# Performance work log

Measured on AMD Instinct MI355X. Metric: run time of the kernel, lower is better.

## Reference

```python
import jax, jax.numpy as jnp
import numpy as np

B, S, D = 2, 1024, 4096          # batch, prefill seqlen, model dim
H, KVH, HD = 32, 8, 128          # q heads, kv heads, head dim
MAX = 2048                       # kv-cache capacity
THETA = 1000000.0
REP = H // KVH


def _rope_tables(pos):
    # pos: [S] int -> cos/sin [S, HD]
    inv_freq = 1.0 / (THETA ** (jnp.arange(0, HD, 2, dtype=jnp.float32) / HD))
    freqs = pos[:, None].astype(jnp.float32) * inv_freq[None, :]
    emb = jnp.concatenate([freqs, freqs], axis=-1)
    return jnp.cos(emb), jnp.sin(emb)


def _rotate_half(t):
    t1, t2 = jnp.split(t, 2, axis=-1)
    return jnp.concatenate([-t2, t1], axis=-1)


def setup_inputs() -> dict:
    key = jax.random.key(0)
    k = jax.random.split(key, 8)
    sc = 1.0 / np.sqrt(D)
    x = jax.random.normal(k[0], (B, S, D), jnp.float32)
    storage_idx = jnp.arange(S, dtype=jnp.int32)
    cache = jnp.zeros((2, 1, B, KVH, MAX, HD), jnp.float32)
    causal = jnp.tril(jnp.ones((MAX, MAX), bool))
    mask = jnp.where(causal, 0.0, -1e9).astype(jnp.float32)
    Wq = jax.random.normal(k[1], (D, H * HD), jnp.float32) * sc
    bq = jax.random.normal(k[2], (H * HD,), jnp.float32) * 0.01
    Wk = jax.random.normal(k[3], (D, KVH * HD), jnp.float32) * sc
    bk = jax.random.normal(k[4], (KVH * HD,), jnp.float32) * 0.01
    Wv = jax.random.normal(k[5], (D, KVH * HD), jnp.float32) * sc
    bv = jax.random.normal(k[6], (KVH * HD,), jnp.float32) * 0.01
    Wo = jax.random.normal(k[7], (H * HD, D), jnp.float32) * sc
    return {"x": x, "storage_idx": storage_idx, "cache": cache, "mask": mask,
            "Wq": Wq, "bq": bq, "Wk": Wk, "bk": bk, "Wv": Wv, "bv": bv, "Wo": Wo}


def reference(x, storage_idx, cache, mask, Wq, bq, Wk, bk, Wv, bv, Wo):
    bsz, seqlen, _ = x.shape
    # QKV projections -> [b, heads, s, hd]
    xq = (x @ Wq + bq).reshape(bsz, seqlen, H, HD).transpose(0, 2, 1, 3)
    xk = (x @ Wk + bk).reshape(bsz, seqlen, KVH, HD).transpose(0, 2, 1, 3)
    xv = (x @ Wv + bv).reshape(bsz, seqlen, KVH, HD).transpose(0, 2, 1, 3)
    # inline RoPE at positions storage_idx
    cos, sin = _rope_tables(storage_idx)       # [s, hd]
    cos = cos[None, None]                      # [1,1,s,hd]
    sin = sin[None, None]
    xq = xq * cos + _rotate_half(xq) * sin
    xk = xk * cos + _rotate_half(xk) * sin
    # KV-cache scatter (index_copy_ on dim -2 at storage_idx)
    keys = cache[0, 0].at[:, :, storage_idx, :].set(xk)    # [b, kvh, MAX, hd]
    values = cache[1, 0].at[:, :, storage_idx, :].set(xv)
    # GQA: repeat kv heads
    keys = jnp.repeat(keys, REP, axis=1)       # [b, H, MAX, hd]
    values = jnp.repeat(values, REP, axis=1)
    # attention with additive mask rows gathered at storage_idx
    scores = jnp.einsum('bhqd,bhkd->bhqk', xq, keys) / np.sqrt(HD)
    scores = scores + mask[storage_idx][None, None]        # [b, H, s, MAX]
    attn = jax.nn.softmax(scores, axis=-1)
    out = jnp.einsum('bhqk,bhkd->bhqd', attn, values)
    out = out.transpose(0, 2, 1, 3).reshape(bsz, seqlen, H * HD)
    return out @ Wo
```

## Files before the change

kernel.cpp:

```cpp
#include <hip/hip_runtime.h>
#include <hip/hip_bf16.h>

typedef unsigned short u16;
typedef unsigned int   u32;
using bf16x8 = __attribute__((ext_vector_type(8))) short;
using f32x4  = __attribute__((ext_vector_type(4))) float;

#define AS1 __attribute__((address_space(1)))
#define AS3 __attribute__((address_space(3)))

static constexpr int S_   = 1024;
static constexpr int D_   = 4096;
static constexpr int H_   = 32;
static constexpr int KVH_ = 8;
static constexpr int HD_  = 128;
static constexpr int NQKV = H_*HD_ + 2*KVH_*HD_;

__device__ __forceinline__ u16 f2bf(float f) {
  union { float f; u32 u; } v; v.f = f;
  u32 r = v.u + 0x7FFFu + ((v.u >> 16) & 1u);
  return (u16)(r >> 16);
}

__global__ void k_convert(const float* __restrict__ src, u16* __restrict__ dst, int n4) {
  int i = blockIdx.x * blockDim.x + threadIdx.x;
  if (i >= n4) return;
  float4 v = ((const float4*)src)[i];
  ushort4 o;
  o.x = f2bf(v.x); o.y = f2bf(v.y); o.z = f2bf(v.z); o.w = f2bf(v.w);
  ((ushort4*)dst)[i] = o;
}

__global__ void k_transpose_w(const float* __restrict__ src, u16* __restrict__ dst,
                              int K, int N) {
  __shared__ float t[32][33];
  int k0 = blockIdx.y * 32, n0 = blockIdx.x * 32;
  int tx = threadIdx.x, ty = threadIdx.y;
#pragma unroll
  for (int i = 0; i < 4; ++i)
    t[ty + i*8][tx] = src[(size_t)(k0 + ty + i*8) * N + n0 + tx];
  __syncthreads();
#pragma unroll
  for (int i = 0; i < 4; ++i)
    dst[(size_t)(n0 + ty + i*8) * K + k0 + tx] = f2bf(t[tx][ty + i*8]);
}

__global__ void k_transpose_v(const u16* __restrict__ src, u16* __restrict__ dst) {
  __shared__ u16 t[32][33];
  int bg = blockIdx.z;
  int s0 = blockIdx.x * 32, h0 = blockIdx.y * 32;
  src += (size_t)bg * S_ * HD_;
  dst += (size_t)bg * S_ * HD_;
  int tx = threadIdx.x, ty = threadIdx.y;
#pragma unroll
  for (int i = 0; i < 4; ++i)
    t[ty + i*8][tx] = src[(size_t)(s0 + ty + i*8) * HD_ + h0 + tx];
  __syncthreads();
#pragma unroll
  for (int i = 0; i < 4; ++i)
    dst[(size_t)(h0 + ty + i*8) * S_ + s0 + tx] = t[tx][ty + i*8];
}

__global__ void k_rope(const int* __restrict__ sidx, float* __restrict__ cosd,
                       float* __restrict__ sind) {
  int i = blockIdx.x * blockDim.x + threadIdx.x;
  int s = i >> 6, d = i & 63;
  float pos  = (float)sidx[s];
  float invf = expf(-0.21586735246819178f * (float)d);
  float ph   = pos * invf;
  cosd[i] = cosf(ph);
  sind[i] = sinf(ph);
}

#define BAR   __builtin_amdgcn_s_barrier()
#define SCHB  __builtin_amdgcn_sched_barrier(0)

__global__ __launch_bounds__(512, 2) void k_gemmq(
    const u16* __restrict__ A, const u16* __restrict__ Bt,
    const float* __restrict__ bq, const float* __restrict__ bk,
    const float* __restrict__ bv,
    const float* __restrict__ cosd, const float* __restrict__ sind,
    u16* __restrict__ qb, u16* __restrict__ kb, u16* __restrict__ vb)
{
  constexpr int K = 4096;
  constexpr int ABYT = 256*128, BBYT = 256*128, STEP = ABYT+BBYT;
  __shared__ __align__(16) char lds[2*STEP];

  const int cpx = (int)gridDim.x >> 3;
  const int wkid = ((int)blockIdx.x & 7)*cpx + ((int)blockIdx.x >> 3);
  const int NT = 24;
  const int m0 = (wkid / NT) * 256, n0 = (wkid % NT) * 256;
  const int tid = threadIdx.x, w = tid>>6, lane = tid&63;
  const int l15 = lane&15, l4 = lane>>4;
  const int wr = w>>1, wc = w&1;
  const int row0 = tid>>3;
  const int ss = (tid&7) ^ (row0&7);
  const int NK = K >> 6;

  f32x4 acc[4][8];
#pragma unroll
  for (int i = 0; i < 4; ++i)
#pragma unroll
    for (int j = 0; j < 8; ++j) acc[i][j] = (f32x4){0.f,0.f,0.f,0.f};

  bf16x8 af[2][2][2];
  bf16x8 bfr[2][4][2];

#define QCHUNK(kt_, part_, r0c_)                                              \
  __builtin_amdgcn_global_load_lds(                                           \
    (AS1 void*)(((part_) ? Bt + (size_t)(n0 + (r0c_) + row0)*K                \
                         : A  + (size_t)(m0 + (r0c_) + row0)*K)               \
                + (size_t)(kt_)*64 + ss*8),                                   \
    (AS3 void*)(lds + ((kt_)&1)*STEP + (part_)*ABYT + (r0c_)*128 + w*1024),   \
    16, 0, 0)

#define QR_A(mh_, lA_)                                                        \
  _Pragma("unroll") for (int i2 = 0; i2 < 2; ++i2)                            \
  _Pragma("unroll") for (int kk = 0; kk < 2; ++kk) {                          \
    int row = wr*64 + ((mh_)*2 + i2)*16 + l15;                                \
    af[mh_][i2][kk] = *(const bf16x8*)((lA_) + row*128 + (((kk*4+l4) ^ (row&7)) << 4)); }

#define QR_B(nh_, lB_)                                                        \
  _Pragma("unroll") for (int jj = 0; jj < 4; ++jj)                            \
  _Pragma("unroll") for (int kk = 0; kk < 2; ++kk) {                          \
    int row = wc*128 + ((nh_)*4 + jj)*16 + l15;                               \
    bfr[nh_][jj][kk] = *(const bf16x8*)((lB_) + row*128 + (((kk*4+l4) ^ (row&7)) << 4)); }

#define QMFMA(mh_, nh_)                                                       \
  __builtin_amdgcn_s_setprio(1);                                              \
  _Pragma("unroll") for (int i2 = 0; i2 < 2; ++i2)                            \
  _Pragma("unroll") for (int jj = 0; jj < 4; ++jj)                            \
  _Pragma("unroll") for (int kk = 0; kk < 2; ++kk)                            \
    acc[(mh_)*2+i2][(nh_)*4+jj] = __builtin_amdgcn_mfma_f32_16x16x32_bf16(    \
        af[mh_][i2][kk], bfr[nh_][jj][kk], acc[(mh_)*2+i2][(nh_)*4+jj], 0, 0, 0); \
  __builtin_amdgcn_s_setprio(0);

  QCHUNK(0,0,0); QCHUNK(0,0,64); QCHUNK(0,0,128); QCHUNK(0,0,192);
  QCHUNK(0,1,0); QCHUNK(0,1,64); QCHUNK(0,1,128); QCHUNK(0,1,192);
  QCHUNK(1,0,0); QCHUNK(1,0,64); QCHUNK(1,0,128); QCHUNK(1,0,192);
  QCHUNK(1,1,0); QCHUNK(1,1,64); QCHUNK(1,1,128); QCHUNK(1,1,192);
  asm volatile("s_waitcnt vmcnt(8)" ::: "memory");
  BAR; SCHB;
  {
    const char* lA0 = lds;
    const char* lB0 = lds + ABYT;
    QR_A(0, lA0); QR_B(0, lB0);
  }

  for (int kt = 0; kt < NK; ++kt) {
    const char* lA = lds + (kt&1)*STEP;
    const char* lB = lA + ABYT;
    QR_B(1, lB);
    asm volatile("s_waitcnt lgkmcnt(8)" ::: "memory");
    SCHB;
    QMFMA(0,0);
    QR_A(1, lA);
    asm volatile("s_waitcnt lgkmcnt(4)" ::: "memory");
    BAR; SCHB;
    if (kt+2 < NK) { QCHUNK(kt+2,1,0); QCHUNK(kt+2,1,64); QCHUNK(kt+2,1,128); QCHUNK(kt+2,1,192); }
    QMFMA(0,1);
    asm volatile("s_waitcnt lgkmcnt(0)" ::: "memory");
    BAR; SCHB;
    if (kt+2 < NK) { QCHUNK(kt+2,0,0); QCHUNK(kt+2,0,64); QCHUNK(kt+2,0,128); QCHUNK(kt+2,0,192); }
    QMFMA(1,0);
    if (kt+1 < NK) {
      if (kt+2 < NK) asm volatile("s_waitcnt vmcnt(8)" ::: "memory");
      else           asm volatile("s_waitcnt vmcnt(0)" ::: "memory");
      BAR; SCHB;
      const char* lAn = lds + ((kt+1)&1)*STEP;
      const char* lBn = lAn + ABYT;
      QR_A(0, lAn); QR_B(0, lBn);
      SCHB;
    }
    QMFMA(1,1);
  }
#undef QCHUNK
#undef QR_A
#undef QR_B
#undef QMFMA

  const int btype = (n0 >= H_*HD_) + (n0 >= H_*HD_ + KVH_*HD_);
  const int colbase = n0 + wc*128 - (btype==1 ? H_*HD_ : btype==2 ? H_*HD_+KVH_*HD_ : 0);
  const int hloc = colbase >> 7;
  const float* bias = btype==0 ? bq : btype==1 ? bk : bv;
  u16* dst = btype==0 ? qb : btype==1 ? kb : vb;
  const int nheads = btype==0 ? H_ : KVH_;
  const float scale = btype==0 ? 0.08838834764831845f : 1.0f;

  float bb[8];
#pragma unroll
  for (int j = 0; j < 8; ++j) bb[j] = bias[colbase + j*16 + l15];

#pragma unroll
  for (int i = 0; i < 4; ++i)
#pragma unroll
    for (int r = 0; r < 4; ++r) {
      int sr = m0 + wr*64 + i*16 + l4*4 + r;
      int b_ = sr >> 10, s_ = sr & 1023;
      size_t obase = (((size_t)b_*nheads + hloc)*S_ + s_)*(size_t)HD_;
      if (btype < 2) {
#pragma unroll
        for (int j = 0; j < 4; ++j) {
          float cs = cosd[s_*64 + j*16 + l15];
          float sn = sind[s_*64 + j*16 + l15];
          float lo = acc[i][j][r]   + bb[j];
          float hi = acc[i][j+4][r] + bb[j+4];
          dst[obase + j*16 + l15]      = f2bf((lo*cs - hi*sn) * scale);
          dst[obase + 64 + j*16 + l15] = f2bf((hi*cs + lo*sn) * scale);
        }
      } else {
#pragma unroll
        for (int j = 0; j < 8; ++j)
          dst[obase + j*16 + l15] = f2bf(acc[i][j][r] + bb[j]);
      }
    }
}

__global__ __launch_bounds__(512, 2) void k_gemmo(
    const u16* __restrict__ A, const u16* __restrict__ Bt,
    float* __restrict__ C, int N, int K)
{
  constexpr int ABYT = 256*128, BBYT = 128*128, STEP = ABYT+BBYT;
  __shared__ __align__(16) char lds[2*STEP];

  const int cpx = (int)gridDim.x >> 3;
  const int wkid = ((int)blockIdx.x & 7)*cpx + ((int)blockIdx.x >> 3);
  const int NT = N / 128;
  const int m0 = (wkid / NT) * 256, n0 = (wkid % NT) * 128;
  const int tid = threadIdx.x, w = tid>>6, lane = tid&63;
  const int l15 = lane&15, l4 = lane>>4;
  const int wr = w>>2, wc = w&3;
  const int row0 = tid>>3;
  const int ss = (tid&7) ^ (row0&7);
  const int NK = K >> 6;

  f32x4 acc[8][2];
#pragma unroll
  for (int i = 0; i < 8; ++i)
#pragma unroll
    for (int j = 0; j < 2; ++j) acc[i][j] = (f32x4){0.f,0.f,0.f,0.f};

  bf16x8 af[2][4][2];
  bf16x8 bfr[2][2];

#define OCHUNK(kt_, part_, r0c_)                                              \
  __builtin_amdgcn_global_load_lds(                                           \
    (AS1 void*)(((part_) ? Bt + (size_t)(n0 + (r0c_) + row0)*K                \
                         : A  + (size_t)(m0 + (r0c_) + row0)*K)               \
                + (size_t)(kt_)*64 + ss*8),                                   \
    (AS3 void*)(lds + ((kt_)&1)*STEP + (part_)*ABYT + (r0c_)*128 + w*1024),   \
    16, 0, 0)

#define OR_A(mh_, lA_)                                                        \
  _Pragma("unroll") for (int i = 0; i < 4; ++i)                               \
  _Pragma("unroll") for (int kk = 0; kk < 2; ++kk) {                          \
    int row = wr*128 + ((mh_)*4 + i)*16 + l15;                                \
    af[mh_][i][kk] = *(const bf16x8*)((lA_) + row*128 + (((kk*4+l4) ^ (row&7)) << 4)); }

#define OR_B(nh_, lB_)                                                        \
  _Pragma("unroll") for (int kk = 0; kk < 2; ++kk) {                          \
    int row = wc*32 + (nh_)*16 + l15;                                         \
    bfr[nh_][kk] = *(const bf16x8*)((lB_) + row*128 + (((kk*4+l4) ^ (row&7)) << 4)); }

#define OMFMA(mh_, nh_)                                                       \
  __builtin_amdgcn_s_setprio(1);                                              \
  _Pragma("unroll") for (int i = 0; i < 4; ++i)                               \
  _Pragma("unroll") for (int kk = 0; kk < 2; ++kk)                            \
    acc[(mh_)*4+i][nh_] = __builtin_amdgcn_mfma_f32_16x16x32_bf16(            \
        af[mh_][i][kk], bfr[nh_][kk], acc[(mh_)*4+i][nh_], 0, 0, 0);          \
  __builtin_amdgcn_s_setprio(0);

  OCHUNK(0,0,0); OCHUNK(0,0,64); OCHUNK(0,0,128); OCHUNK(0,0,192);
  OCHUNK(0,1,0); OCHUNK(0,1,64);
  OCHUNK(1,0,0); OCHUNK(1,0,64); OCHUNK(1,0,128); OCHUNK(1,0,192);
  OCHUNK(1,1,0); OCHUNK(1,1,64);
  asm volatile("s_waitcnt vmcnt(6)" ::: "memory");
  BAR; SCHB;
  {
    const char* lA0 = lds;
    const char* lB0 = lds + ABYT;
    OR_A(0, lA0); OR_B(0, lB0);
  }

  for (int kt = 0; kt < NK; ++kt) {
    const char* lA = lds + (kt&1)*STEP;
    const char* lB = lA + ABYT;
    OR_B(1, lB);
    asm volatile("s_waitcnt lgkmcnt(2)" ::: "memory");
    SCHB;
    OMFMA(0,0);
    OR_A(1, lA);
    asm volatile("s_waitcnt lgkmcnt(8)" ::: "memory");
    BAR; SCHB;
    if (kt+2 < NK) { OCHUNK(kt+2,1,0); OCHUNK(kt+2,1,64); }
    OMFMA(0,1);
    asm volatile("s_waitcnt lgkmcnt(0)" ::: "memory");
    BAR; SCHB;
    if (kt+2 < NK) { OCHUNK(kt+2,0,0); OCHUNK(kt+2,0,64); OCHUNK(kt+2,0,128); OCHUNK(kt+2,0,192); }
    OMFMA(1,0);
    if (kt+1 < NK) {
      if (kt+2 < NK) asm volatile("s_waitcnt vmcnt(6)" ::: "memory");
      else           asm volatile("s_waitcnt vmcnt(0)" ::: "memory");
      BAR; SCHB;
      const char* lAn = lds + ((kt+1)&1)*STEP;
      const char* lBn = lAn + ABYT;
      OR_A(0, lAn); OR_B(0, lBn);
      SCHB;
    }
    OMFMA(1,1);
  }
#undef OCHUNK
#undef OR_A
#undef OR_B
#undef OMFMA

#pragma unroll
  for (int i = 0; i < 8; ++i)
#pragma unroll
    for (int j = 0; j < 2; ++j) {
      int r0 = m0 + wr*128 + i*16 + l4*4;
      int c0 = n0 + wc*32 + j*16 + l15;
#pragma unroll
      for (int r = 0; r < 4; ++r)
        C[(size_t)(r0 + r) * N + c0] = acc[i][j][r];
    }
}

__global__ __launch_bounds__(256, 4) void k_attn(
    const u16* __restrict__ Q, const u16* __restrict__ Kc,
    const u16* __restrict__ Vt, u16* __restrict__ AO)
{
  __shared__ __align__(16) char Kls[2][16384];
  __shared__ __align__(16) char Vls[2][16384];
  __shared__ u16 Pl[4][1024];

  int id = blockIdx.x;
  int slot = id >> 3;
  int bg   = (id & 7)*2 + (slot & 1);
  int rem  = slot >> 1;
  int h_in = rem & 3, bx = rem >> 2;
  int b = bg >> 3, g = bg & 7, h = g*4 + h_in;
  int tA = bx, tB = 15 - bx;

  int tid = threadIdx.x, w = tid >> 6, lane = tid & 63;
  int l15 = lane & 15, l4 = lane >> 4;
  const u16* Qh = Q  + ((size_t)b*H_   + h) * S_ * HD_;
  const u16* Kp = Kc + ((size_t)b*KVH_ + g) * S_ * HD_;
  const u16* Vp = Vt + ((size_t)b*KVH_ + g) * (size_t)HD_ * S_;
  u16* AOh = AO + ((size_t)b*S_) * (H_*HD_) + h*HD_;
  char* Pw = (char*)&Pl[w][0];

  int kOff[4], vOff[4];
#pragma unroll
  for (int c = 0; c < 4; ++c) {
    int ci = c*256 + tid;
    int krow = ci >> 4, ks = ci & 15;
    kOff[c] = krow * HD_ + ((ks & 8) | ((ks & 7) ^ (krow & 7))) * 8;
    int vrow = ci >> 3, vs = ci & 7;
    vOff[c] = vrow * S_ + (vs ^ (vrow & 7)) * 8;
  }

#define ASTAGE(kv_, bb_) {                                                    \
    const u16* ks_ = Kp + (size_t)(kv_) * 64 * HD_;                           \
    const u16* vs_ = Vp + (size_t)(kv_) * 64;                                 \
    _Pragma("unroll") for (int c = 0; c < 4; ++c) {                           \
      __builtin_amdgcn_global_load_lds((AS1 void*)(ks_ + kOff[c]),            \
          (AS3 void*)(&Kls[bb_][0] + c*4096 + w*1024), 16, 0, 0);             \
      __builtin_amdgcn_global_load_lds((AS1 void*)(vs_ + vOff[c]),            \
          (AS3 void*)(&Vls[bb_][0] + c*4096 + w*1024), 16, 0, 0); } }

  bf16x8 qf[4];
#pragma unroll
  for (int kc = 0; kc < 4; ++kc)
    qf[kc] = *(const bf16x8*)(Qh + (size_t)(tA*64 + w*16 + l15)*HD_ + kc*32 + l4*8);

  f32x4 o[8];
#pragma unroll
  for (int n = 0; n < 8; ++n) o[n] = (f32x4){0.f,0.f,0.f,0.f};
  float mrow[4] = {-3e38f,-3e38f,-3e38f,-3e38f};
  float lrow[4] = {0.f,0.f,0.f,0.f};

  ASTAGE(0, 0);
  asm volatile("s_waitcnt vmcnt(0)" ::: "memory");
  __builtin_amdgcn_s_barrier();

  const int NIT = tA + tB + 2;
  int buf = 0;
  for (int it = 0; it < NIT; ++it) {
    bool phA = (it <= tA);
    int kv = phA ? it : it - tA - 1;
    int qt = phA ? tA : tB;
    if (it + 1 < NIT) {
      int kvn = (it + 1 <= tA) ? it + 1 : it - tA;
      ASTAGE(kvn, buf ^ 1);
    }
    const char* Ksb = &Kls[buf][0];
    const char* Vsb = &Vls[buf][0];

    f32x4 sc[4];
    __builtin_amdgcn_s_setprio(1);
#pragma unroll
    for (int ct = 0; ct < 4; ++ct) {
      f32x4 s4 = (f32x4){0.f,0.f,0.f,0.f};
#pragma unroll
      for (int kc = 0; kc < 4; ++kc) {
        int row = ct*16 + l15, s = kc*4 + l4;
        bf16x8 kf = *(const bf16x8*)(Ksb + row*256 + ((((s & 7) ^ (row & 7)) | (s & 8)) << 4));
        s4 = __builtin_amdgcn_mfma_f32_16x16x32_bf16(qf[kc], kf, s4, 0, 0, 0);
      }
      sc[ct] = s4;
    }
    __builtin_amdgcn_s_setprio(0);

    if (kv == qt) {
      int qrow0 = qt*64 + w*16;
#pragma unroll
      for (int ct = 0; ct < 4; ++ct)
#pragma unroll
        for (int r = 0; r < 4; ++r) {
          int col = kv*64 + ct*16 + l15;
          if (col > qrow0 + l4*4 + r) sc[ct][r] = -1e9f;
        }
    }

    float f[4];
#pragma unroll
    for (int r = 0; r < 4; ++r) {
      float mx = fmaxf(fmaxf(sc[0][r], sc[1][r]), fmaxf(sc[2][r], sc[3][r]));
      mx = fmaxf(mx, __shfl_xor(mx, 1));
      mx = fmaxf(mx, __shfl_xor(mx, 2));
      mx = fmaxf(mx, __shfl_xor(mx, 4));
      mx = fmaxf(mx, __shfl_xor(mx, 8));
      float nm = fmaxf(mrow[r], mx);
      f[r] = __expf(mrow[r] - nm);
      mrow[r] = nm;
    }
    float rs[4] = {0.f,0.f,0.f,0.f};
#pragma unroll
    for (int ct = 0; ct < 4; ++ct)
#pragma unroll
      for (int r = 0; r < 4; ++r) {
        float p = __expf(sc[ct][r] - mrow[r]);
        rs[r] += p;
        int row = l4*4 + r, col = ct*16 + l15;
        int byte = row*128 + (((col >> 3) ^ (row & 7)) << 4) + (col & 7)*2;
        *(u16*)(Pw + byte) = f2bf(p);
      }
#pragma unroll
    for (int r = 0; r < 4; ++r) {
      float sum = rs[r];
      sum += __shfl_xor(sum, 1);
      sum += __shfl_xor(sum, 2);
      sum += __shfl_xor(sum, 4);
      sum += __shfl_xor(sum, 8);
      lrow[r] = lrow[r]*f[r] + sum;
    }
#pragma unroll
    for (int n = 0; n < 8; ++n)
#pragma unroll
      for (int r = 0; r < 4; ++r) o[n][r] *= f[r];

    __builtin_amdgcn_s_setprio(1);
#pragma unroll
    for (int kk = 0; kk < 2; ++kk) {
      int pbyte = l15*128 + (((kk*4 + l4) ^ (l15 & 7)) << 4);
      bf16x8 pf = *(const bf16x8*)(Pw + pbyte);
#pragma unroll
      for (int n = 0; n < 8; ++n) {
        int vrow = n*16 + l15, s = kk*4 + l4;
        bf16x8 vf = *(const bf16x8*)(Vsb + vrow*128 + ((s ^ (vrow & 7)) << 4));
        o[n] = __builtin_amdgcn_mfma_f32_16x16x32_bf16(pf, vf, o[n], 0, 0, 0);
      }
    }
    __builtin_amdgcn_s_setprio(0);

    if (it == tA) {
#pragma unroll
      for (int n = 0; n < 8; ++n)
#pragma unroll
        for (int r = 0; r < 4; ++r) {
          int srow = tA*64 + w*16 + l4*4 + r;
          AOh[(size_t)srow * (H_*HD_) + n*16 + l15] = f2bf(o[n][r] / lrow[r]);
        }
#pragma unroll
      for (int n = 0; n < 8; ++n) o[n] = (f32x4){0.f,0.f,0.f,0.f};
#pragma unroll
      for (int r = 0; r < 4; ++r) { mrow[r] = -3e38f; lrow[r] = 0.f; }
#pragma unroll
      for (int kc = 0; kc < 4; ++kc)
        qf[kc] = *(const bf16x8*)(Qh + (size_t)(tB*64 + w*16 + l15)*HD_ + kc*32 + l4*8);
    }

    asm volatile("s_waitcnt vmcnt(0)" ::: "memory");
    __builtin_amdgcn_s_barrier();
    buf ^= 1;
  }
#undef ASTAGE

#pragma unroll
  for (int n = 0; n < 8; ++n)
#pragma unroll
    for (int r = 0; r < 4; ++r) {
      int srow = tB*64 + w*16 + l4*4 + r;
      AOh[(size_t)srow * (H_*HD_) + n*16 + l15] = f2bf(o[n][r] / lrow[r]);
    }
}

extern "C" void kernel_launch(void* const* d_in, const int* in_sizes, int n_in,
                              void* d_out, int out_size, void* d_ws, size_t ws_size,
                              hipStream_t stream) {
  (void)in_sizes; (void)n_in; (void)out_size; (void)ws_size;
  const float* x   = (const float*)d_in[0];
  const int*   sid = (const int*)  d_in[1];
  const float* Wq  = (const float*)d_in[4];
  const float* bq  = (const float*)d_in[5];
  const float* Wk  = (const float*)d_in[6];
  const float* bk  = (const float*)d_in[7];
  const float* Wv  = (const float*)d_in[8];
  const float* bv  = (const float*)d_in[9];
  const float* Wo  = (const float*)d_in[10];
  float* out = (float*)d_out;

  char* ws = (char*)d_ws;
  u16*   xb   = (u16*)  (ws);
  u16*   WB   = (u16*)  (ws + 16777216);
  u16*   WoT  = (u16*)  (ws + 67108864);
  u16*   qb   = (u16*)  (ws + 150994944);
  u16*   kb   = (u16*)  (ws + 167772160);
  u16*   vb   = (u16*)  (ws + 171966464);
  u16*   VT   = (u16*)  (ws + 176160768);
  float* cosd = (float*)(ws + 180355072);
  float* sind = (float*)(ws + 180617216);
  u16*   AO   = xb;

  dim3 tb(32, 8);
  k_convert<<<8192, 256, 0, stream>>>(x, xb, (2048*4096)/4);
  k_transpose_w<<<dim3(128,128), tb, 0, stream>>>(Wq, WB, 4096, 4096);
  k_transpose_w<<<dim3( 32,128), tb, 0, stream>>>(Wk, WB + (size_t)4096*4096, 4096, 1024);
  k_transpose_w<<<dim3( 32,128), tb, 0, stream>>>(Wv, WB + (size_t)5120*4096, 4096, 1024);
  k_transpose_w<<<dim3(128,128), tb, 0, stream>>>(Wo, WoT, 4096, 4096);
  k_rope<<<256, 256, 0, stream>>>(sid, cosd, sind);
  k_gemmq<<<192, 512, 0, stream>>>(xb, WB, bq, bk, bv, cosd, sind, qb, kb, vb);
  k_transpose_v<<<dim3(32,4,16), tb, 0, stream>>>(vb, VT);
  k_attn<<<512, 256, 0, stream>>>(qb, kb, VT, AO);
  k_gemmo<<<256, 512, 0, stream>>>(AO, WoT, out, 4096, 4096);
}
```

Before: 294.0 us.

## Vectorize weight transpose with 64x64 tiles and reshape output GEMM tile

The weight transpose now uses 64x64 tiles with float4 global reads and 8-wide packed bf16 writes, cutting memory transactions in a pass that moves large fp32 weights. The output projection GEMM block tile changes from 256x128 to 128x256, with each wave computing a 64x64 sub-tile instead of 128x32. This should give each wave better fragment reuse and a different load split, with lgkmcnt waits adjusted to match. The LDS transpose writes of four consecutive rows per thread may cause bank conflicts. The wait counts must also match the new load counts exactly, or reads could race.

Result: faster. 286.4 us (-2.6%).

```diff
diff --git a/kernel.cpp b/kernel.cpp
--- a/kernel.cpp
+++ b/kernel.cpp
@@ -31,18 +31,34 @@
   ((ushort4*)dst)[i] = o;
 }
 
-__global__ void k_transpose_w(const float* __restrict__ src, u16* __restrict__ dst,
-                              int K, int N) {
-  __shared__ float t[32][33];
-  int k0 = blockIdx.y * 32, n0 = blockIdx.x * 32;
-  int tx = threadIdx.x, ty = threadIdx.y;
-#pragma unroll
-  for (int i = 0; i < 4; ++i)
-    t[ty + i*8][tx] = src[(size_t)(k0 + ty + i*8) * N + n0 + tx];
+__global__ __launch_bounds__(256) void k_transpose_w(
+    const float* __restrict__ src, u16* __restrict__ dst, int K, int N) {
+  __shared__ float t[64][65];
+  int k0 = blockIdx.y * 64, n0 = blockIdx.x * 64;
+  int tid = threadIdx.x;
+  int lr = tid >> 4;
+  int lc = (tid & 15) * 4;
+#pragma unroll
+  for (int i = 0; i < 4; ++i) {
+    float4 v = *(const float4*)&src[(size_t)(k0 + lr + i*16) * N + n0 + lc];
+    t[lc+0][lr + i*16] = v.x;
+    t[lc+1][lr + i*16] = v.y;
+    t[lc+2][lr + i*16] = v.z;
+    t[lc+3][lr + i*16] = v.w;
+  }
   __syncthreads();
-#pragma unroll
-  for (int i = 0; i < 4; ++i)
-    dst[(size_t)(n0 + ty + i*8) * K + k0 + tx] = f2bf(t[tx][ty + i*8]);
+  int wn = tid >> 3;
+  int wk = (tid & 7) * 8;
+#pragma unroll
+  for (int i = 0; i < 2; ++i) {
+    const float* row = &t[wn + i*32][wk];
+    ushort4 a, b;
+    a.x = f2bf(row[0]); a.y = f2bf(row[1]); a.z = f2bf(row[2]); a.w = f2bf(row[3]);
+    b.x = f2bf(row[4]); b.y = f2bf(row[5]); b.z = f2bf(row[6]); b.w = f2bf(row[7]);
+    u16* o = &dst[(size_t)(n0 + wn + i*32) * K + k0 + wk];
+    *(ushort4*)o = a;
+    *(ushort4*)(o + 4) = b;
+  }
 }
 
 __global__ void k_transpose_v(const u16* __restrict__ src, u16* __restrict__ dst) {
@@ -220,13 +236,13 @@
     const u16* __restrict__ A, const u16* __restrict__ Bt,
     float* __restrict__ C, int N, int K)
 {
-  constexpr int ABYT = 256*128, BBYT = 128*128, STEP = ABYT+BBYT;
+  constexpr int ABYT = 128*128, BBYT = 256*128, STEP = ABYT+BBYT;
   __shared__ __align__(16) char lds[2*STEP];
 
   const int cpx = (int)gridDim.x >> 3;
   const int wkid = ((int)blockIdx.x & 7)*cpx + ((int)blockIdx.x >> 3);
-  const int NT = N / 128;
-  const int m0 = (wkid / NT) * 256, n0 = (wkid % NT) * 128;
+  const int NT = N / 256;
+  const int m0 = (wkid / NT) * 128, n0 = (wkid % NT) * 256;
   const int tid = threadIdx.x, w = tid>>6, lane = tid&63;
   const int l15 = lane&15, l4 = lane>>4;
   const int wr = w>>2, wc = w&3;
@@ -234,14 +250,14 @@
   const int ss = (tid&7) ^ (row0&7);
   const int NK = K >> 6;
 
-  f32x4 acc[8][2];
-#pragma unroll
-  for (int i = 0; i < 8; ++i)
-#pragma unroll
-    for (int j = 0; j < 2; ++j) acc[i][j] = (f32x4){0.f,0.f,0.f,0.f};
-
-  bf16x8 af[2][4][2];
-  bf16x8 bfr[2][2];
+  f32x4 acc[4][4];
+#pragma unroll
+  for (int i = 0; i < 4; ++i)
+#pragma unroll
+    for (int j = 0; j < 4; ++j) acc[i][j] = (f32x4){0.f,0.f,0.f,0.f};
+
+  bf16x8 af[2][2][2];
+  bf16x8 bfr[2][2][2];
 
 #define OCHUNK(kt_, part_, r0c_)                                              \
   __builtin_amdgcn_global_load_lds(                                           \
@@ -252,28 +268,30 @@
     16, 0, 0)
 
 #define OR_A(mh_, lA_)                                                        \
-  _Pragma("unroll") for (int i = 0; i < 4; ++i)                               \
+  _Pragma("unroll") for (int i2 = 0; i2 < 2; ++i2)                            \
   _Pragma("unroll") for (int kk = 0; kk < 2; ++kk) {                          \
-    int row = wr*128 + ((mh_)*4 + i)*16 + l15;                                \
-    af[mh_][i][kk] = *(const bf16x8*)((lA_) + row*128 + (((kk*4+l4) ^ (row&7)) << 4)); }
+    int row = wr*64 + ((mh_)*2 + i2)*16 + l15;                                \
+    af[mh_][i2][kk] = *(const bf16x8*)((lA_) + row*128 + (((kk*4+l4) ^ (row&7)) << 4)); }
 
 #define OR_B(nh_, lB_)                                                        \
+  _Pragma("unroll") for (int j2 = 0; j2 < 2; ++j2)                            \
   _Pragma("unroll") for (int kk = 0; kk < 2; ++kk) {                          \
-    int row = wc*32 + (nh_)*16 + l15;                                         \
-    bfr[nh_][kk] = *(const bf16x8*)((lB_) + row*128 + (((kk*4+l4) ^ (row&7)) << 4)); }
+    int row = wc*64 + ((nh_)*2 + j2)*16 + l15;                                \
+    bfr[nh_][j2][kk] = *(const bf16x8*)((lB_) + row*128 + (((kk*4+l4) ^ (row&7)) << 4)); }
 
 #define OMFMA(mh_, nh_)                                                       \
   __builtin_amdgcn_s_setprio(1);                                              \
-  _Pragma("unroll") for (int i = 0; i < 4; ++i)                               \
+  _Pragma("unroll") for (int i2 = 0; i2 < 2; ++i2)                            \
+  _Pragma("unroll") for (int j2 = 0; j2 < 2; ++j2)                            \
   _Pragma("unroll") for (int kk = 0; kk < 2; ++kk)                            \
-    acc[(mh_)*4+i][nh_] = __builtin_amdgcn_mfma_f32_16x16x32_bf16(            \
-        af[mh_][i][kk], bfr[nh_][kk], acc[(mh_)*4+i][nh_], 0, 0, 0);          \
+    acc[(mh_)*2+i2][(nh_)*2+j2] = __builtin_amdgcn_mfma_f32_16x16x32_bf16(    \
+        af[mh_][i2][kk], bfr[nh_][j2][kk], acc[(mh_)*2+i2][(nh_)*2+j2], 0, 0, 0); \
   __builtin_amdgcn_s_setprio(0);
 
-  OCHUNK(0,0,0); OCHUNK(0,0,64); OCHUNK(0,0,128); OCHUNK(0,0,192);
-  OCHUNK(0,1,0); OCHUNK(0,1,64);
-  OCHUNK(1,0,0); OCHUNK(1,0,64); OCHUNK(1,0,128); OCHUNK(1,0,192);
-  OCHUNK(1,1,0); OCHUNK(1,1,64);
+  OCHUNK(0,0,0); OCHUNK(0,0,64);
+  OCHUNK(0,1,0); OCHUNK(0,1,64); OCHUNK(0,1,128); OCHUNK(0,1,192);
+  OCHUNK(1,0,0); OCHUNK(1,0,64);
+  OCHUNK(1,1,0); OCHUNK(1,1,64); OCHUNK(1,1,128); OCHUNK(1,1,192);
   asm volatile("s_waitcnt vmcnt(6)" ::: "memory");
   BAR; SCHB;
   {
@@ -286,17 +304,17 @@
     const char* lA = lds + (kt&1)*STEP;
     const char* lB = lA + ABYT;
     OR_B(1, lB);
-    asm volatile("s_waitcnt lgkmcnt(2)" ::: "memory");
+    asm volatile("s_waitcnt lgkmcnt(4)" ::: "memory");
     SCHB;
     OMFMA(0,0);
     OR_A(1, lA);
-    asm volatile("s_waitcnt lgkmcnt(8)" ::: "memory");
+    asm volatile("s_waitcnt lgkmcnt(4)" ::: "memory");
     BAR; SCHB;
-    if (kt+2 < NK) { OCHUNK(kt+2,1,0); OCHUNK(kt+2,1,64); }
+    if (kt+2 < NK) { OCHUNK(kt+2,1,0); OCHUNK(kt+2,1,64); OCHUNK(kt+2,1,128); OCHUNK(kt+2,1,192); }
     OMFMA(0,1);
     asm volatile("s_waitcnt lgkmcnt(0)" ::: "memory");
     BAR; SCHB;
-    if (kt+2 < NK) { OCHUNK(kt+2,0,0); OCHUNK(kt+2,0,64); OCHUNK(kt+2,0,128); OCHUNK(kt+2,0,192); }
+    if (kt+2 < NK) { OCHUNK(kt+2,0,0); OCHUNK(kt+2,0,64); }
     OMFMA(1,0);
     if (kt+1 < NK) {
       if (kt+2 < NK) asm volatile("s_waitcnt vmcnt(6)" ::: "memory");
@@ -315,11 +333,11 @@
 #undef OMFMA
 
 #pragma unroll
-  for (int i = 0; i < 8; ++i)
-#pragma unroll
-    for (int j = 0; j < 2; ++j) {
-      int r0 = m0 + wr*128 + i*16 + l4*4;
-      int c0 = n0 + wc*32 + j*16 + l15;
+  for (int i = 0; i < 4; ++i)
+#pragma unroll
+    for (int j = 0; j < 4; ++j) {
+      int r0 = m0 + wr*64 + i*16 + l4*4;
+      int c0 = n0 + wc*64 + j*16 + l15;
 #pragma unroll
       for (int r = 0; r < 4; ++r)
         C[(size_t)(r0 + r) * N + c0] = acc[i][j][r];
@@ -535,10 +553,10 @@
 
   dim3 tb(32, 8);
   k_convert<<<8192, 256, 0, stream>>>(x, xb, (2048*4096)/4);
-  k_transpose_w<<<dim3(128,128), tb, 0, stream>>>(Wq, WB, 4096, 4096);
-  k_transpose_w<<<dim3( 32,128), tb, 0, stream>>>(Wk, WB + (size_t)4096*4096, 4096, 1024);
-  k_transpose_w<<<dim3( 32,128), tb, 0, stream>>>(Wv, WB + (size_t)5120*4096, 4096, 1024);
-  k_transpose_w<<<dim3(128,128), tb, 0, stream>>>(Wo, WoT, 4096, 4096);
+  k_transpose_w<<<dim3(64,64), 256, 0, stream>>>(Wq, WB, 4096, 4096);
+  k_transpose_w<<<dim3(16,64), 256, 0, stream>>>(Wk, WB + (size_t)4096*4096, 4096, 1024);
+  k_transpose_w<<<dim3(16,64), 256, 0, stream>>>(Wv, WB + (size_t)5120*4096, 4096, 1024);
+  k_transpose_w<<<dim3(64,64), 256, 0, stream>>>(Wo, WoT, 4096, 4096);
   k_rope<<<256, 256, 0, stream>>>(sid, cosd, sind);
   k_gemmq<<<192, 512, 0, stream>>>(xb, WB, bq, bk, bv, cosd, sind, qb, kb, vb);
   k_transpose_v<<<dim3(32,4,16), tb, 0, stream>>>(vb, VT);
```
